# Kernel tuning notes

Measured on AMD Instinct MI355X. Metric: run time of the kernel, lower is better.

The kernel has to match this reference:

```python
import jax, jax.numpy as jnp
import numpy as np

B, C, N, K, H = 8, 64, 4096, 32, 4
D = C // H  # head dim = 16
EPS = 1e-5  # BatchNorm eps (torch default)


def setup_inputs() -> dict:
    key = jax.random.key(0)
    ks = jax.random.split(key, 7)
    s = 0.05
    return {
        "x": jax.random.normal(ks[0], (B, C, N), jnp.float32),
        "wq": jax.random.normal(ks[1], (C, C), jnp.float32) * s,
        "wk": jax.random.normal(ks[2], (C, C), jnp.float32) * s,
        "wv": jax.random.normal(ks[3], (C, C), jnp.float32) * s,
        "w1": jax.random.normal(ks[4], (4 * C, C), jnp.float32) * s,
        "w2": jax.random.normal(ks[5], (C, 4 * C), jnp.float32) * s,
        "g1": jnp.ones((C,), jnp.float32),
        "b1": jnp.zeros((C,), jnp.float32),
        "g2": jnp.ones((C,), jnp.float32),
        "b2": jnp.zeros((C,), jnp.float32),
    }


def _bn(f, g, b):
    # BatchNorm1d in training mode: stats over (batch, points) per channel.
    # f: (B, N, C)
    mu = jnp.mean(f, axis=(0, 1))
    var = jnp.var(f, axis=(0, 1))  # biased, as torch uses for normalization
    return (f - mu) * jax.lax.rsqrt(var + EPS) * g + b


def reference(x, wq, wk, wv, w1, w2, g1, b1, g2, b2):
    feat = jnp.transpose(x, (0, 2, 1))  # (B, N, C)
    # KNN in feature space: negative squared distances, take top-K largest
    sq = jnp.sum(feat * feat, axis=-1)  # (B, N)
    neg_d = 2.0 * jnp.einsum('bnc,bmc->bnm', feat, feat) - sq[:, :, None] - sq[:, None, :]
    _, idx = jax.lax.top_k(neg_d, K)  # (B, N, K) int32
    # gather neighbors and form diffs
    nbrs = jax.vmap(lambda p, i: p[i])(feat, idx)  # (B, N, K, C)
    diff = nbrs - feat[:, :, None, :]
    # 1x1-conv projections (bias-free linear over channels)
    q = jnp.einsum('bnc,oc->bno', feat, wq).reshape(B, N, H, D)
    k = jnp.einsum('bnkc,oc->bnko', diff, wk).reshape(B, N, K, H, D)
    v = jnp.einsum('bnkc,oc->bnko', diff, wv).reshape(B, N, K, H, D)
    energy = jnp.einsum('bnhd,bnkhd->bnhk', q, k) / jnp.sqrt(jnp.float32(D))
    attn = jax.nn.softmax(energy, axis=-1)  # softmax over K neighbors
    out = jnp.einsum('bnhk,bnkhd->bnhd', attn, v).reshape(B, N, C)  # H-major merge
    f1 = _bn(feat + out, g1, b1)
    hid = jnp.einsum('bnc,oc->bno', f1, w1)
    hid = jnp.where(hid > 0, hid, 0.2 * hid)  # LeakyReLU(0.2)
    ff = jnp.einsum('bno,co->bnc', hid, w2)
    f2 = _bn(f1 + ff, g2, b2)
    return jnp.transpose(f2, (0, 2, 1))  # (B, C, N)
```

## Files before the change

kernel.cpp:

```cpp
#include <hip/hip_runtime.h>

#define Bdim 8
#define Cdim 64
#define Ndim 4096
#define Kdim 32
#define ROWS (Bdim*Ndim)
#define BN_EPS 1e-5f

__device__ __forceinline__ float dot4(float4 a, float4 b){
  return a.x*b.x + a.y*b.y + a.z*b.z + a.w*b.w;
}
__device__ __forceinline__ int wofs(int o, int g){ return o*64 + (((g ^ ((o>>2)&7)))<<2); }
__device__ __forceinline__ unsigned keyOf(float f){
  unsigned u = __float_as_uint(f);
  return (u & 0x80000000u) ? ~u : (u ^ 0x80000000u);
}

__global__ __launch_bounds__(256) void prep_proj_kernel(const float* __restrict__ x,
    const float* __restrict__ wq, const float* __restrict__ wk,
    const float* __restrict__ wv,
    float* __restrict__ sq,
    float* __restrict__ Qo, float* __restrict__ PKo, float* __restrict__ PVo,
    float* __restrict__ accZ)
{
  __shared__ __align__(16) float ftile[64*68];
  __shared__ __align__(16) float Ws[3][64*64];
  const int tid = threadIdx.x;
  const int blk = blockIdx.x;
  const int b  = blk & 7;
  const int n0 = (blk >> 3) * 64;
  if (blk == 0) accZ[tid] = 0.f;
  for (int k=0;k<16;++k){
    int idx = tid + (k<<8);
    int c = idx>>6, nn = idx&63;
    ftile[nn*68+c] = x[((size_t)b*64+c)*Ndim + n0 + nn];
  }
  {
    const float* wp[3] = {wq, wk, wv};
    for (int m=0;m<3;++m)
      for (int k=0;k<16;++k){
        int idx = tid + (k<<8);
        int o = idx>>6, c = idx&63;
        Ws[m][wofs(o, c>>2) + (c&3)] = wp[m][o*64 + c];
      }
  }
  __syncthreads();
  if (tid < 64){
    float a = 0.f;
    #pragma unroll
    for (int c=0;c<64;++c){ float v = ftile[tid*68+c]; a += v*v; }
    sq[b*Ndim + n0 + tid] = a;
  }
  const int tr = tid>>4, to = tid&15;
  const size_t rowBase = (size_t)b*Ndim + n0;
  float* outp[3] = {Qo, PKo, PVo};
  for (int m=0;m<3;++m){
    float acc[4][4];
    #pragma unroll
    for (int r=0;r<4;++r){ acc[r][0]=0.f; acc[r][1]=0.f; acc[r][2]=0.f; acc[r][3]=0.f; }
    #pragma unroll 4
    for (int c4=0;c4<16;++c4){
      float4 f[4], w[4];
      #pragma unroll
      for (int r=0;r<4;++r)  f[r] = *(const float4*)&ftile[(4*tr+r)*68 + (c4<<2)];
      #pragma unroll
      for (int oo=0;oo<4;++oo) w[oo] = *(const float4*)&Ws[m][wofs(4*to+oo, c4)];
      #pragma unroll
      for (int r=0;r<4;++r)
        #pragma unroll
        for (int oo=0;oo<4;++oo)
          acc[r][oo] += dot4(f[r], w[oo]);
    }
    #pragma unroll
    for (int r=0;r<4;++r){
      float4 v; v.x=acc[r][0]; v.y=acc[r][1]; v.z=acc[r][2]; v.w=acc[r][3];
      *(float4*)&outp[m][(rowBase + 4*tr + r)*64 + 4*to] = v;
    }
  }
}

__global__ __launch_bounds__(512, 4) void knn_attn_kernel(
    const float* __restrict__ x,
    const float* __restrict__ sq,
    const float* __restrict__ Qm, const float* __restrict__ PKm, const float* __restrict__ PVm,
    float* __restrict__ t1, float* __restrict__ bn1s, float* __restrict__ bn1q)
{
  __shared__ __align__(16) unsigned char smem[40992];
  float*    chunkF = (float*)smem;
  unsigned* candK  = (unsigned*)smem;
  int*      candI  = (int*)(smem + 2048);
  int*      outIdx = (int*)(smem + 4096);
  float*    enS    = (float*)(smem + 5120);
  float*    red1   = (float*)(smem + 5120);
  float*    red2   = (float*)(smem + 7168);
  float*    fnS    = (float*)(smem + 32768);
  float*    qvS    = (float*)(smem + 34816);
  float*    pknS   = (float*)(smem + 36864);
  float*    pvnS   = (float*)(smem + 38912);
  float*    sqnS   = (float*)(smem + 40960);

  const int tid = threadIdx.x;
  const int lane = tid & 63;
  const int w = tid >> 6;
  const int blk = blockIdx.x;
  const int b  = blk & 7;
  const int n0 = (blk >> 3) << 3;
  const float* xb = x + (size_t)b*64*Ndim;

  {
    int j = tid>>6, c = tid&63;
    size_t ro = ((size_t)b*Ndim + n0 + j)*64 + c;
    fnS[tid]  = xb[(size_t)c*Ndim + n0 + j];
    qvS[tid]  = Qm[ro];
    pknS[tid] = PKm[ro];
    pvnS[tid] = PVm[ro];
    if (tid < 8) sqnS[tid] = sq[b*Ndim + n0 + tid];
  }
  __syncthreads();

  unsigned kk[64];

  #pragma unroll
  for (int g=0; g<2; ++g){
    const int m0 = (g<<11) + (tid<<2);
    float acc[8][4];
    #pragma unroll
    for (int q=0;q<8;++q){ acc[q][0]=0.f; acc[q][1]=0.f; acc[q][2]=0.f; acc[q][3]=0.f; }
    #pragma unroll 4
    for (int c=0;c<64;++c){
      float4 xm = *(const float4*)&xb[(size_t)c*Ndim + m0];
      float4 qA = *(const float4*)&xb[(size_t)c*Ndim + n0];
      float4 qB = *(const float4*)&xb[(size_t)c*Ndim + n0 + 4];
      const float qs[8] = {qA.x,qA.y,qA.z,qA.w,qB.x,qB.y,qB.z,qB.w};
      #pragma unroll
      for (int q=0;q<8;++q){
        acc[q][0] += qs[q]*xm.x; acc[q][1] += qs[q]*xm.y;
        acc[q][2] += qs[q]*xm.z; acc[q][3] += qs[q]*xm.w;
      }
    }
    float4 sqm4 = *(const float4*)&sq[b*Ndim + m0];
    #pragma unroll
    for (int half=0; half<2; ++half){
      __syncthreads();
      #pragma unroll
      for (int qq=0;qq<4;++qq){
        int q = (half<<2)+qq;
        float sqn_q = sqnS[q];
        float4 v;
        v.x = (2.f*acc[q][0]-sqn_q)-sqm4.x;
        v.y = (2.f*acc[q][1]-sqn_q)-sqm4.y;
        v.z = (2.f*acc[q][2]-sqn_q)-sqm4.z;
        v.w = (2.f*acc[q][3]-sqn_q)-sqm4.w;
        *(float4*)&chunkF[(qq<<11) + (tid<<2)] = v;
      }
      __syncthreads();
      if ((w>>2) == half){
        const int wq = w & 3;
        #pragma unroll
        for (int i=0;i<32;++i)
          kk[(g<<5)+i] = keyOf(chunkF[(wq<<11)+(i<<6)+lane]);
      }
    }
  }
  __syncthreads();

  if (lane < 32) outIdx[(w<<5)+lane] = n0 + w;

  {
    unsigned lmax = kk[0];
    #pragma unroll
    for (int j=1;j<64;++j) lmax = lmax > kk[j] ? lmax : kk[j];
    unsigned T = 0u;
    #pragma unroll
    for (int bit=31; bit>=0; --bit){
      unsigned cand = T | (1u << bit);
      int cnt = (int)__popcll(__ballot(lmax >= cand));
      if (cnt >= 32) T = cand;
    }
    int base = 0;
    #pragma unroll
    for (int j=0;j<64;++j){
      bool isc = (kk[j] >= T);
      unsigned long long mk = __ballot(isc);
      if (isc){
        int slot = base + (int)__popcll(mk & ((1ull<<lane)-1ull));
        if (slot < 64){
          candK[(w<<6)+slot] = kk[j];
          candI[(w<<6)+slot] = ((j>>5)<<11)+((j&31)<<6)+lane;
        }
      }
      base += (int)__popcll(mk);
    }
    const int S = base;
    __threadfence_block();
    if (S <= 64){
      unsigned long long C = 0ull;
      if (lane < S)
        C = ((unsigned long long)candK[(w<<6)+lane] << 32) |
            (unsigned long long)(~(unsigned)candI[(w<<6)+lane]);
      #pragma unroll
      for (int k2=2; k2<=64; k2<<=1){
        #pragma unroll
        for (int j2=k2>>1; j2>=1; j2>>=1){
          unsigned long long P = (unsigned long long)__shfl_xor((long long)C, j2, 64);
          bool lowIdx  = ((lane & j2) == 0);
          bool keepMax = (lowIdx == ((lane & k2) == 0));
          unsigned long long mx = C > P ? C : P;
          unsigned long long mn = C > P ? P : C;
          C = keepMax ? mx : mn;
        }
      }
      if (lane < 32) outIdx[(w<<5)+lane] = (int)(~(unsigned)(C & 0xFFFFFFFFull)) & (Ndim-1);
    } else {
      unsigned Te = 0u;
      for (int bit=31; bit>=0; --bit){
        unsigned cand = Te | (1u << bit);
        int lc = 0;
        #pragma unroll
        for (int j=0;j<64;++j) lc += (kk[j] >= cand) ? 1 : 0;
        #pragma unroll
        for (int off=1; off<64; off<<=1) lc += __shfl_xor(lc, off, 64);
        if (lc >= 32) Te = cand;
      }
      const unsigned long long below = (1ull << lane) - 1ull;
      int b2 = 0;
      #pragma unroll
      for (int j=0;j<64;++j){
        unsigned u = kk[j];
        unsigned long long mg = __ballot(u > Te);
        if (u > Te){
          int slot = b2 + (int)__popcll(mg & below);
          if (slot < 32) outIdx[(w<<5)+slot] = ((j>>5)<<11)+((j&31)<<6)+lane;
        }
        b2 += (int)__popcll(mg);
      }
      #pragma unroll
      for (int j=0;j<64;++j){
        unsigned u = kk[j];
        unsigned long long mt = __ballot(u == Te);
        if (u == Te){
          int slot = b2 + (int)__popcll(mt & below);
          if (slot < 32) outIdx[(w<<5)+slot] = ((j>>5)<<11)+((j&31)<<6)+lane;
        }
        b2 += (int)__popcll(mt);
      }
    }
  }
  __syncthreads();

  #pragma unroll
  for (int p=0;p<2;++p){
    int task = tid + (p<<9);
    int jn = task>>7, h = (task>>5)&3, k2 = task&31;
    int mj = outIdx[(jn<<5)+k2] & (Ndim-1);
    const float4* pk4 = (const float4*)(PKm + ((size_t)b*Ndim + mj)*64 + (h<<4));
    const float4* qq4 = (const float4*)&qvS[(jn<<6)+(h<<4)];
    const float4* nn4 = (const float4*)&pknS[(jn<<6)+(h<<4)];
    float e = 0.f;
    #pragma unroll
    for (int d=0;d<4;++d){
      float4 kv = pk4[d], qq = qq4[d], nn = nn4[d];
      e += qq.x*(kv.x-nn.x) + qq.y*(kv.y-nn.y) + qq.z*(kv.z-nn.z) + qq.w*(kv.w-nn.w);
    }
    enS[(jn<<7)+(h<<5)+k2] = e * 0.25f;
  }
  __syncthreads();
  if (tid < 32){
    int jn = tid>>2, h = tid&3;
    float* ep = &enS[(jn<<7)+(h<<5)];
    float mx = -1e30f;
    for (int k2=0;k2<32;++k2) mx = fmaxf(mx, ep[k2]);
    float ssum = 0.f;
    for (int k2=0;k2<32;++k2){ float ex = expf(ep[k2]-mx); ep[k2] = ex; ssum += ex; }
    float inv = 1.f/ssum;
    for (int k2=0;k2<32;++k2) ep[k2] *= inv;
  }
  __syncthreads();
  float tval;
  {
    int jn = tid>>6, c = tid&63, h = c>>4;
    float a2 = 0.f;
    #pragma unroll 8
    for (int k2=0;k2<32;++k2){
      int mj = outIdx[(jn<<5)+k2] & (Ndim-1);
      a2 += enS[(jn<<7)+(h<<5)+k2] * (PVm[((size_t)b*Ndim + mj)*64 + c] - pvnS[(jn<<6)+c]);
    }
    tval = fnS[(jn<<6)+c] + a2;
    t1[((size_t)b*Ndim + n0 + jn)*64 + c] = tval;
  }
  __syncthreads();
  red1[tid] = tval;
  red2[tid] = tval*tval;
  __syncthreads();
  if (tid < 64){
    float S = 0.f, S2 = 0.f;
    #pragma unroll
    for (int j=0;j<8;++j){ S += red1[(j<<6)+tid]; S2 += red2[(j<<6)+tid]; }
    atomicAdd(&bn1s[tid], S);
    atomicAdd(&bn1q[tid], S2);
  }
}

__global__ __launch_bounds__(256) void mlp_kernel(const float* __restrict__ t1,
    const float* __restrict__ w1, const float* __restrict__ w2,
    const float* __restrict__ g1, const float* __restrict__ b1,
    const float* __restrict__ bns, const float* __restrict__ bnq,
    float* __restrict__ t2, float* __restrict__ bn2s, float* __restrict__ bn2q)
{
  __shared__ __align__(16) float f1l[64*68];
  __shared__ __align__(16) float hl[64*68];
  __shared__ __align__(16) float w1s[64*64];
  __shared__ __align__(16) float w2s[64*64];
  __shared__ float mu[64], rs[64], gg[64], bb[64];
  const int tid = threadIdx.x;
  if (tid < 64){
    float m = bns[tid] * (1.f/32768.f);
    float v = bnq[tid] * (1.f/32768.f) - m*m;
    mu[tid] = m; rs[tid] = 1.f/sqrtf(v + BN_EPS);
    gg[tid] = g1[tid]; bb[tid] = b1[tid];
  }
  __syncthreads();
  const size_t rowBase = (size_t)blockIdx.x*64;
  for (int k=0;k<16;++k){
    int idx = tid + (k<<8);
    int r = idx>>6, c = idx&63;
    float v = t1[(rowBase + r)*64 + c];
    f1l[r*68+c] = (v - mu[c])*rs[c]*gg[c] + bb[c];
  }
  const int tr = tid>>4, to = tid&15;
  float ff[4][4];
  #pragma unroll
  for (int r=0;r<4;++r){ ff[r][0]=0.f; ff[r][1]=0.f; ff[r][2]=0.f; ff[r][3]=0.f; }

  for (int hc=0; hc<4; ++hc){
    __syncthreads();
    for (int k=0;k<16;++k){
      int idx = tid + (k<<8);
      int o = idx>>6, c = idx&63;
      w1s[wofs(o, c>>2) + (c&3)] = w1[(size_t)(hc*64+o)*64 + c];
      w2s[wofs(o, c>>2) + (c&3)] = w2[(size_t)o*256 + hc*64 + c];
    }
    __syncthreads();
    float hv[4][4];
    #pragma unroll
    for (int r=0;r<4;++r){ hv[r][0]=0.f; hv[r][1]=0.f; hv[r][2]=0.f; hv[r][3]=0.f; }
    #pragma unroll 4
    for (int c4=0;c4<16;++c4){
      float4 f[4], w[4];
      #pragma unroll
      for (int r=0;r<4;++r)  f[r] = *(const float4*)&f1l[(4*tr+r)*68 + (c4<<2)];
      #pragma unroll
      for (int oo=0;oo<4;++oo) w[oo] = *(const float4*)&w1s[wofs(4*to+oo, c4)];
      #pragma unroll
      for (int r=0;r<4;++r)
        #pragma unroll
        for (int oo=0;oo<4;++oo)
          hv[r][oo] += dot4(f[r], w[oo]);
    }
    #pragma unroll
    for (int r=0;r<4;++r){
      float4 v;
      float x0=hv[r][0], x1=hv[r][1], x2=hv[r][2], x3=hv[r][3];
      v.x = (x0>0.f)?x0:0.2f*x0; v.y = (x1>0.f)?x1:0.2f*x1;
      v.z = (x2>0.f)?x2:0.2f*x2; v.w = (x3>0.f)?x3:0.2f*x3;
      *(float4*)&hl[(4*tr+r)*68 + 4*to] = v;
    }
    __syncthreads();
    #pragma unroll 4
    for (int o4=0;o4<16;++o4){
      float4 h[4], w[4];
      #pragma unroll
      for (int r=0;r<4;++r)  h[r] = *(const float4*)&hl[(4*tr+r)*68 + (o4<<2)];
      #pragma unroll
      for (int oo=0;oo<4;++oo) w[oo] = *(const float4*)&w2s[wofs(4*to+oo, o4)];
      #pragma unroll
      for (int r=0;r<4;++r)
        #pragma unroll
        for (int oo=0;oo<4;++oo)
          ff[r][oo] += dot4(h[r], w[oo]);
    }
  }
  float ls[4]  = {0.f,0.f,0.f,0.f};
  float ls2[4] = {0.f,0.f,0.f,0.f};
  #pragma unroll
  for (int r=0;r<4;++r){
    float4 v;
    v.x = f1l[(4*tr+r)*68 + 4*to+0] + ff[r][0];
    v.y = f1l[(4*tr+r)*68 + 4*to+1] + ff[r][1];
    v.z = f1l[(4*tr+r)*68 + 4*to+2] + ff[r][2];
    v.w = f1l[(4*tr+r)*68 + 4*to+3] + ff[r][3];
    *(float4*)&t2[(rowBase + 4*tr + r)*64 + 4*to] = v;
    ls[0]+=v.x; ls[1]+=v.y; ls[2]+=v.z; ls[3]+=v.w;
    ls2[0]+=v.x*v.x; ls2[1]+=v.y*v.y; ls2[2]+=v.z*v.z; ls2[3]+=v.w*v.w;
  }
  __syncthreads();
  #pragma unroll
  for (int i=0;i<4;++i){
    hl[tr*64 + 4*to + i]        = ls[i];
    hl[1024 + tr*64 + 4*to + i] = ls2[i];
  }
  __syncthreads();
  if (tid < 64){
    float S = 0.f, S2 = 0.f;
    #pragma unroll
    for (int g2=0; g2<16; ++g2){ S += hl[g2*64 + tid]; S2 += hl[1024 + g2*64 + tid]; }
    atomicAdd(&bn2s[tid], S);
    atomicAdd(&bn2q[tid], S2);
  }
}

__global__ __launch_bounds__(256) void final_kernel(const float* __restrict__ t2,
    const float* __restrict__ bns, const float* __restrict__ bnq,
    const float* __restrict__ g2, const float* __restrict__ b2,
    float* __restrict__ out)
{
  __shared__ float tile[64*65];
  __shared__ float mu[64], rs[64], gg[64], bb[64];
  const int tid = threadIdx.x;
  const int b = blockIdx.y;
  const int n0 = blockIdx.x*64;
  if (tid < 64){
    float m = bns[tid] * (1.f/32768.f);
    float v = bnq[tid] * (1.f/32768.f) - m*m;
    mu[tid] = m; rs[tid] = 1.f/sqrtf(v + BN_EPS);
    gg[tid] = g2[tid]; bb[tid] = b2[tid];
  }
  __syncthreads();
  for (int k=0;k<16;++k){
    int idx = tid + (k<<8);
    int r = idx>>6, c = idx&63;
    float v = t2[((size_t)b*Ndim + n0 + r)*64 + c];
    tile[r*65+c] = (v - mu[c])*rs[c]*gg[c] + bb[c];
  }
  __syncthreads();
  for (int k=0;k<16;++k){
    int idx = tid + (k<<8);
    int c = idx>>6, nn = idx&63;
    out[((size_t)b*64 + c)*Ndim + n0 + nn] = tile[nn*65+c];
  }
}

extern "C" void kernel_launch(void* const* d_in, const int* in_sizes, int n_in,
                              void* d_out, int out_size, void* d_ws, size_t ws_size,
                              hipStream_t stream)
{
  (void)in_sizes; (void)n_in; (void)out_size; (void)ws_size;
  const float* x  = (const float*)d_in[0];
  const float* wq = (const float*)d_in[1];
  const float* wk = (const float*)d_in[2];
  const float* wv = (const float*)d_in[3];
  const float* w1 = (const float*)d_in[4];
  const float* w2 = (const float*)d_in[5];
  const float* g1 = (const float*)d_in[6];
  const float* b1 = (const float*)d_in[7];
  const float* g2 = (const float*)d_in[8];
  const float* b2 = (const float*)d_in[9];
  float* out = (float*)d_out;

  const size_t NE = (size_t)ROWS*64;
  float* sq   = (float*)d_ws;
  float* Qb   = sq + ROWS;
  float* PKb  = Qb + NE;
  float* PVb  = PKb + NE;
  float* t1   = PVb + NE;
  float* t2   = t1 + NE;
  float* acc  = t2 + NE;

  prep_proj_kernel<<<dim3(512), 256, 0, stream>>>(x, wq, wk, wv, sq, Qb, PKb, PVb, acc);
  knn_attn_kernel<<<dim3(4096), 512, 0, stream>>>(x, sq, Qb, PKb, PVb, t1, acc, acc+64);
  mlp_kernel<<<dim3(512), 256, 0, stream>>>(t1, w1, w2, g1, b1, acc, acc+64, t2, acc+128, acc+192);
  final_kernel<<<dim3(64,8), 256, 0, stream>>>(t2, acc+128, acc+192, g2, b2, out);
}
```

Baseline: 444.9 us.

## Compute KNN distances with split-bf16 MFMA and rescore candidates in fp32

The prep kernel now writes hi/lo bf16 splits of the point features in an MFMA-friendly tiled layout. The KNN kernel uses 16x16x32 bf16 MFMA with three split products (hi*hi, hi*lo, lo*hi) to approximate the pairwise dot products, instead of scalar fp32 FMAs. The threshold is widened to about 36-64 candidates, which are then rescored exactly in fp32 and sorted with a bitonic network. This offloads the dominant distance GEMM to matrix cores at the cost of a larger shared-memory footprint (lower occupancy), extra bf16 buffers stored in the t2 workspace, and a per-candidate gather rescore.

Measured after the change: 720.9 us. +62.0%, slower.

```diff
diff --git a/kernel.cpp b/kernel.cpp
--- a/kernel.cpp
+++ b/kernel.cpp
@@ -7,6 +7,9 @@
 #define ROWS (Bdim*Ndim)
 #define BN_EPS 1e-5f
 
+typedef __attribute__((ext_vector_type(8))) short s8v;
+typedef __attribute__((ext_vector_type(4))) float f4v;
+
 __device__ __forceinline__ float dot4(float4 a, float4 b){
   return a.x*b.x + a.y*b.y + a.z*b.z + a.w*b.w;
 }
@@ -14,6 +17,10 @@
 __device__ __forceinline__ unsigned keyOf(float f){
   unsigned u = __float_as_uint(f);
   return (u & 0x80000000u) ? ~u : (u ^ 0x80000000u);
+}
+__device__ __forceinline__ unsigned bfhi(float f){
+  unsigned u = __float_as_uint(f);
+  return (u + 0x7FFFu + ((u>>16)&1u)) >> 16;
 }
 
 __global__ __launch_bounds__(256) void prep_proj_kernel(const float* __restrict__ x,
@@ -21,7 +28,7 @@
     const float* __restrict__ wv,
     float* __restrict__ sq,
     float* __restrict__ Qo, float* __restrict__ PKo, float* __restrict__ PVo,
-    float* __restrict__ accZ)
+    float* __restrict__ accZ, short* __restrict__ Ph, short* __restrict__ Pl)
 {
   __shared__ __align__(16) float ftile[64*68];
   __shared__ __align__(16) float Ws[3][64*64];
@@ -51,6 +58,27 @@
     for (int c=0;c<64;++c){ float v = ftile[tid*68+c]; a += v*v; }
     sq[b*Ndim + n0 + tid] = a;
   }
+  {
+    const int mtBase = n0 >> 4;
+    #pragma unroll
+    for (int s=0;s<2;++s){
+      int slot = tid + (s<<8);
+      int mt = slot>>7, k8 = (slot>>4)&7, nn2 = slot&15;
+      const float* src = &ftile[(mt*16+nn2)*68 + (k8<<3)];
+      s8v h8, l8;
+      #pragma unroll
+      for (int j2=0;j2<8;++j2){
+        float f = src[j2];
+        unsigned hr = bfhi(f);
+        float fh = __uint_as_float(hr<<16);
+        unsigned lr2 = bfhi(f - fh);
+        h8[j2] = (short)hr; l8[j2] = (short)lr2;
+      }
+      size_t off = ((((size_t)b<<8) + (size_t)(mtBase + mt))<<10) + (k8<<7) + (nn2<<3);
+      *(s8v*)(Ph + off) = h8;
+      *(s8v*)(Pl + off) = l8;
+    }
+  }
   const int tr = tid>>4, to = tid&15;
   const size_t rowBase = (size_t)b*Ndim + n0;
   float* outp[3] = {Qo, PKo, PVo};
@@ -83,21 +111,23 @@
     const float* __restrict__ x,
     const float* __restrict__ sq,
     const float* __restrict__ Qm, const float* __restrict__ PKm, const float* __restrict__ PVm,
+    const short* __restrict__ Ph, const short* __restrict__ Pl,
     float* __restrict__ t1, float* __restrict__ bn1s, float* __restrict__ bn1q)
 {
-  __shared__ __align__(16) unsigned char smem[40992];
+  __shared__ __align__(16) unsigned char smem[77888];
   float*    chunkF = (float*)smem;
-  unsigned* candK  = (unsigned*)smem;
-  int*      candI  = (int*)(smem + 2048);
-  int*      outIdx = (int*)(smem + 4096);
-  float*    enS    = (float*)(smem + 5120);
-  float*    red1   = (float*)(smem + 5120);
-  float*    red2   = (float*)(smem + 7168);
-  float*    fnS    = (float*)(smem + 32768);
-  float*    qvS    = (float*)(smem + 34816);
-  float*    pknS   = (float*)(smem + 36864);
-  float*    pvnS   = (float*)(smem + 38912);
-  float*    sqnS   = (float*)(smem + 40960);
+  int*      candI  = (int*)smem;
+  int*      outIdx = (int*)(smem + 2048);
+  float*    enS    = (float*)(smem + 3072);
+  float*    red1   = (float*)(smem + 3072);
+  float*    red2   = (float*)(smem + 5120);
+  short*    qhiL   = (short*)(smem + 65536);
+  short*    qloL   = (short*)(smem + 67584);
+  float*    fnS    = (float*)(smem + 69632);
+  float*    qvS    = (float*)(smem + 71680);
+  float*    pknS   = (float*)(smem + 73728);
+  float*    pvnS   = (float*)(smem + 75776);
+  float*    sqnS   = (float*)(smem + 77824);
 
   const int tid = threadIdx.x;
   const int lane = tid & 63;
@@ -110,61 +140,68 @@
   {
     int j = tid>>6, c = tid&63;
     size_t ro = ((size_t)b*Ndim + n0 + j)*64 + c;
-    fnS[tid]  = xb[(size_t)c*Ndim + n0 + j];
+    float f = xb[(size_t)c*Ndim + n0 + j];
+    fnS[tid]  = f;
     qvS[tid]  = Qm[ro];
     pknS[tid] = PKm[ro];
     pvnS[tid] = PVm[ro];
     if (tid < 8) sqnS[tid] = sq[b*Ndim + n0 + tid];
-  }
-  __syncthreads();
-
+    unsigned hr = bfhi(f);
+    float fh = __uint_as_float(hr<<16);
+    unsigned lr2 = bfhi(f - fh);
+    qhiL[tid] = (short)hr;  qloL[tid] = (short)lr2;
+    qhiL[512 + tid] = 0;    qloL[512 + tid] = 0;
+  }
+  __syncthreads();
+
+  const int qn = lane & 15, quad = lane >> 4;
+  const s8v ah0 = *(const s8v*)&qhiL[qn*64 + quad*8];
+  const s8v ah1 = *(const s8v*)&qhiL[qn*64 + 32 + quad*8];
+  const s8v al0 = *(const s8v*)&qloL[qn*64 + quad*8];
+  const s8v al1 = *(const s8v*)&qloL[qn*64 + 32 + quad*8];
+  float sqn_r[4];
+  #pragma unroll
+  for (int r=0;r<4;++r) sqn_r[r] = sqnS[(quad&1)*4 + r];
+
+  const short* Phb = Ph + ((size_t)b<<18);
+  const short* Plb = Pl + ((size_t)b<<18);
   unsigned kk[64];
 
-  #pragma unroll
   for (int g=0; g<2; ++g){
-    const int m0 = (g<<11) + (tid<<2);
-    float acc[8][4];
-    #pragma unroll
-    for (int q=0;q<8;++q){ acc[q][0]=0.f; acc[q][1]=0.f; acc[q][2]=0.f; acc[q][3]=0.f; }
-    #pragma unroll 4
-    for (int c=0;c<64;++c){
-      float4 xm = *(const float4*)&xb[(size_t)c*Ndim + m0];
-      float4 qA = *(const float4*)&xb[(size_t)c*Ndim + n0];
-      float4 qB = *(const float4*)&xb[(size_t)c*Ndim + n0 + 4];
-      const float qs[8] = {qA.x,qA.y,qA.z,qA.w,qB.x,qB.y,qB.z,qB.w};
-      #pragma unroll
-      for (int q=0;q<8;++q){
-        acc[q][0] += qs[q]*xm.x; acc[q][1] += qs[q]*xm.y;
-        acc[q][2] += qs[q]*xm.z; acc[q][3] += qs[q]*xm.w;
-      }
-    }
-    float4 sqm4 = *(const float4*)&sq[b*Ndim + m0];
-    #pragma unroll
-    for (int half=0; half<2; ++half){
-      __syncthreads();
-      #pragma unroll
-      for (int qq=0;qq<4;++qq){
-        int q = (half<<2)+qq;
-        float sqn_q = sqnS[q];
-        float4 v;
-        v.x = (2.f*acc[q][0]-sqn_q)-sqm4.x;
-        v.y = (2.f*acc[q][1]-sqn_q)-sqm4.y;
-        v.z = (2.f*acc[q][2]-sqn_q)-sqm4.z;
-        v.w = (2.f*acc[q][3]-sqn_q)-sqm4.w;
-        *(float4*)&chunkF[(qq<<11) + (tid<<2)] = v;
-      }
-      __syncthreads();
-      if ((w>>2) == half){
-        const int wq = w & 3;
+    for (int t=0; t<16; ++t){
+      const int mtL = (w<<4) + t;
+      const int mtg = (g<<7) + mtL;
+      const size_t fo = ((size_t)mtg<<10) + (quad<<7) + (qn<<3);
+      s8v bh0 = *(const s8v*)(Phb + fo);
+      s8v bh1 = *(const s8v*)(Phb + fo + 512);
+      s8v bl0 = *(const s8v*)(Plb + fo);
+      s8v bl1 = *(const s8v*)(Plb + fo + 512);
+      f4v D1 = {0.f,0.f,0.f,0.f}, D2 = {0.f,0.f,0.f,0.f};
+      D1 = __builtin_amdgcn_mfma_f32_16x16x32_bf16(ah0, bh0, D1, 0,0,0);
+      D1 = __builtin_amdgcn_mfma_f32_16x16x32_bf16(ah1, bh1, D1, 0,0,0);
+      D2 = __builtin_amdgcn_mfma_f32_16x16x32_bf16(ah0, bl0, D2, 0,0,0);
+      D2 = __builtin_amdgcn_mfma_f32_16x16x32_bf16(ah1, bl1, D2, 0,0,0);
+      D2 = __builtin_amdgcn_mfma_f32_16x16x32_bf16(al0, bh0, D2, 0,0,0);
+      D2 = __builtin_amdgcn_mfma_f32_16x16x32_bf16(al1, bh1, D2, 0,0,0);
+      float sqm = sq[b*Ndim + (mtg<<4) + qn];
+      if (quad < 2){
+        int lm = (mtL<<4) + qn;
         #pragma unroll
-        for (int i=0;i<32;++i)
-          kk[(g<<5)+i] = keyOf(chunkF[(wq<<11)+(i<<6)+lane]);
-      }
-    }
-  }
-  __syncthreads();
+        for (int r=0;r<4;++r){
+          float d = 2.f*(D1[r]+D2[r]) - sqn_r[r] - sqm;
+          chunkF[((quad<<2)+r)*2048 + lm] = d;
+        }
+      }
+    }
+    __syncthreads();
+    #pragma unroll
+    for (int i=0;i<32;++i)
+      kk[(g<<5)+i] = keyOf(chunkF[(w<<11) + (i<<6) + lane]);
+    __syncthreads();
+  }
 
   if (lane < 32) outIdx[(w<<5)+lane] = n0 + w;
+  candI[(w<<6)+lane] = n0 + w;
 
   {
     unsigned lmax = kk[0];
@@ -175,43 +212,21 @@
     for (int bit=31; bit>=0; --bit){
       unsigned cand = T | (1u << bit);
       int cnt = (int)__popcll(__ballot(lmax >= cand));
-      if (cnt >= 32) T = cand;
-    }
-    int base = 0;
+      if (cnt >= 36) T = cand;
+    }
+    const unsigned long long below = (1ull << lane) - 1ull;
+    int S = 0;
     #pragma unroll
     for (int j=0;j<64;++j){
       bool isc = (kk[j] >= T);
       unsigned long long mk = __ballot(isc);
       if (isc){
-        int slot = base + (int)__popcll(mk & ((1ull<<lane)-1ull));
-        if (slot < 64){
-          candK[(w<<6)+slot] = kk[j];
-          candI[(w<<6)+slot] = ((j>>5)<<11)+((j&31)<<6)+lane;
-        }
-      }
-      base += (int)__popcll(mk);
-    }
-    const int S = base;
-    __threadfence_block();
-    if (S <= 64){
-      unsigned long long C = 0ull;
-      if (lane < S)
-        C = ((unsigned long long)candK[(w<<6)+lane] << 32) |
-            (unsigned long long)(~(unsigned)candI[(w<<6)+lane]);
-      #pragma unroll
-      for (int k2=2; k2<=64; k2<<=1){
-        #pragma unroll
-        for (int j2=k2>>1; j2>=1; j2>>=1){
-          unsigned long long P = (unsigned long long)__shfl_xor((long long)C, j2, 64);
-          bool lowIdx  = ((lane & j2) == 0);
-          bool keepMax = (lowIdx == ((lane & k2) == 0));
-          unsigned long long mx = C > P ? C : P;
-          unsigned long long mn = C > P ? P : C;
-          C = keepMax ? mx : mn;
-        }
-      }
-      if (lane < 32) outIdx[(w<<5)+lane] = (int)(~(unsigned)(C & 0xFFFFFFFFull)) & (Ndim-1);
-    } else {
+        int slot = S + (int)__popcll(mk & below);
+        if (slot < 64) candI[(w<<6)+slot] = ((j>>5)<<11)+((j&31)<<6)+lane;
+      }
+      S += (int)__popcll(mk);
+    }
+    if (S > 64){
       unsigned Te = 0u;
       for (int bit=31; bit>=0; --bit){
         unsigned cand = Te | (1u << bit);
@@ -220,9 +235,8 @@
         for (int j=0;j<64;++j) lc += (kk[j] >= cand) ? 1 : 0;
         #pragma unroll
         for (int off=1; off<64; off<<=1) lc += __shfl_xor(lc, off, 64);
-        if (lc >= 32) Te = cand;
-      }
-      const unsigned long long below = (1ull << lane) - 1ull;
+        if (lc >= 64) Te = cand;
+      }
       int b2 = 0;
       #pragma unroll
       for (int j=0;j<64;++j){
@@ -230,21 +244,46 @@
         unsigned long long mg = __ballot(u > Te);
         if (u > Te){
           int slot = b2 + (int)__popcll(mg & below);
-          if (slot < 32) outIdx[(w<<5)+slot] = ((j>>5)<<11)+((j&31)<<6)+lane;
+          if (slot < 64) candI[(w<<6)+slot] = ((j>>5)<<11)+((j&31)<<6)+lane;
         }
         b2 += (int)__popcll(mg);
       }
       #pragma unroll
       for (int j=0;j<64;++j){
         unsigned u = kk[j];
-        unsigned long long mt = __ballot(u == Te);
+        unsigned long long mt2 = __ballot(u == Te);
         if (u == Te){
-          int slot = b2 + (int)__popcll(mt & below);
-          if (slot < 32) outIdx[(w<<5)+slot] = ((j>>5)<<11)+((j&31)<<6)+lane;
+          int slot = b2 + (int)__popcll(mt2 & below);
+          if (slot < 64) candI[(w<<6)+slot] = ((j>>5)<<11)+((j&31)<<6)+lane;
         }
-        b2 += (int)__popcll(mt);
-      }
-    }
+        b2 += (int)__popcll(mt2);
+      }
+      S = 64;
+    }
+    __threadfence_block();
+    unsigned long long C = 0ull;
+    if (lane < S){
+      int mj = candI[(w<<6)+lane] & (Ndim-1);
+      float a0 = 0.f;
+      const float* xmp = xb + mj;
+      #pragma unroll 8
+      for (int c=0;c<64;++c) a0 = fmaf(fnS[(w<<6)+c], xmp[(size_t)c*Ndim], a0);
+      float d = (2.f*a0 - sqnS[w]) - sq[b*Ndim + mj];
+      C = ((unsigned long long)keyOf(d) << 32) | (unsigned long long)(~(unsigned)mj);
+    }
+    #pragma unroll
+    for (int k2=2; k2<=64; k2<<=1){
+      #pragma unroll
+      for (int j2=k2>>1; j2>=1; j2>>=1){
+        unsigned long long P = (unsigned long long)__shfl_xor((long long)C, j2, 64);
+        bool lowIdx  = ((lane & j2) == 0);
+        bool keepMax = (lowIdx == ((lane & k2) == 0));
+        unsigned long long mx = C > P ? C : P;
+        unsigned long long mn = C > P ? P : C;
+        C = keepMax ? mx : mn;
+      }
+    }
+    if (lane < 32) outIdx[(w<<5)+lane] = (int)(~(unsigned)(C & 0xFFFFFFFFull)) & (Ndim-1);
   }
   __syncthreads();
 
@@ -465,9 +504,11 @@
   float* t1   = PVb + NE;
   float* t2   = t1 + NE;
   float* acc  = t2 + NE;
-
-  prep_proj_kernel<<<dim3(512), 256, 0, stream>>>(x, wq, wk, wv, sq, Qb, PKb, PVb, acc);
-  knn_attn_kernel<<<dim3(4096), 512, 0, stream>>>(x, sq, Qb, PKb, PVb, t1, acc, acc+64);
+  short* Ph = (short*)t2;
+  short* Pl = Ph + (size_t)2097152;
+
+  prep_proj_kernel<<<dim3(512), 256, 0, stream>>>(x, wq, wk, wv, sq, Qb, PKb, PVb, acc, Ph, Pl);
+  knn_attn_kernel<<<dim3(4096), 512, 0, stream>>>(x, sq, Qb, PKb, PVb, Ph, Pl, t1, acc, acc+64);
   mlp_kernel<<<dim3(512), 256, 0, stream>>>(t1, w1, w2, g1, b1, acc, acc+64, t2, acc+128, acc+192);
   final_kernel<<<dim3(64,8), 256, 0, stream>>>(t2, acc+128, acc+192, g2, b2, out);
 }
```
